# Optimization experiments

Hardware: AMD Instinct MI355X
Metric: run time of the kernel (lower is better)

The kernel has to match this reference:

```python
import jax, jax.numpy as jnp
import numpy as np

K = 20      # kNN neighbors
H = 4       # attention heads
EPS = 1e-5  # BatchNorm eps
NEG = 0.2   # LeakyReLU negative slope


def lrelu(x):
    return jnp.where(x >= 0, x, NEG * x)


def bn(x, g, b):
    # eval-mode BatchNorm: running_mean=0, running_var=1
    return x * (g / jnp.sqrt(1.0 + EPS)) + b


def knn_idx(x):
    # x: (B, N, C) -> (B, N, K) indices of K nearest neighbors (incl. self)
    inner = -2.0 * jnp.einsum('bnc,bmc->bnm', x, x)
    xx = jnp.sum(x * x, axis=-1)
    pd = -xx[:, :, None] - inner - xx[:, None, :]  # negative squared distance
    return jax.lax.top_k(pd, K)[1]


def edge_conv(x, w, g, b):
    # EdgeConv: gather kNN features, cat(nbr-ctr, ctr), 1x1 conv, BN, LeakyReLU, max over K
    idx = knn_idx(x)                                   # (B,N,K)
    nbr = jax.vmap(lambda f, i: f[i])(x, idx)          # (B,N,K,C)
    ctr = jnp.broadcast_to(x[:, :, None, :], nbr.shape)
    e = jnp.concatenate([nbr - ctr, ctr], axis=-1)     # (B,N,K,2C)
    h = lrelu(bn(jnp.einsum('bnkc,oc->bnko', e, w), g, b))
    return jnp.max(h, axis=2)                          # (B,N,Cout)


def mha(x, w_in, b_in, w_out, b_out):
    # Faithful to source: (B,N,E) fed to nn.MultiheadAttention with batch_first=False,
    # so seq length L=B and batch=N (attention mixes across the batch axis).
    L, Nb, E = x.shape
    d = E // H
    qkv = x @ w_in.T + b_in
    q, k, v = jnp.split(qkv, 3, axis=-1)
    q = q.reshape(L, Nb, H, d) * (1.0 / np.sqrt(d))
    k = k.reshape(L, Nb, H, d)
    v = v.reshape(L, Nb, H, d)
    a = jax.nn.softmax(jnp.einsum('lnhd,mnhd->nhlm', q, k), axis=-1)
    o = jnp.einsum('nhlm,mnhd->lnhd', a, v).reshape(L, Nb, E)
    return o @ w_out.T + b_out


def setup_inputs():
    ks = iter(jax.random.split(jax.random.key(0), 64))
    def rn(shape, s=0.05):
        return jax.random.normal(next(ks), shape, jnp.float32) * s
    def gamma(c):
        return 1.0 + rn((c,), 0.1)
    B, N = 8, 1024
    inp = {'x': rn((B, N, 3), 1.0)}
    for i, (ci, co) in enumerate([(6, 64), (128, 64), (128, 128), (256, 256)], 1):
        inp[f'w{i}'] = rn((co, ci)); inp[f'g{i}'] = gamma(co); inp[f'b{i}'] = rn((co,))
    for i, e in enumerate([64, 64, 128, 256], 1):
        inp[f'a{i}_wi'] = rn((3 * e, e)); inp[f'a{i}_bi'] = rn((3 * e,))
        inp[f'a{i}_wo'] = rn((e, e));     inp[f'a{i}_bo'] = rn((e,))
    inp['w5'] = rn((1024, 512)); inp['g5'] = gamma(1024); inp['b5'] = rn((1024,))
    inp['l1w'] = rn((512, 2048)); inp['g6'] = gamma(512); inp['b6'] = rn((512,))
    inp['l2w'] = rn((256, 512)); inp['l2b'] = rn((256,))
    inp['g7'] = gamma(256); inp['b7'] = rn((256,))
    inp['l3w'] = rn((40, 256)); inp['l3b'] = rn((40,))
    return inp


def reference(x, w1, g1, b1, a1_wi, a1_bi, a1_wo, a1_bo,
              w2, g2, b2, a2_wi, a2_bi, a2_wo, a2_bo,
              w3, g3, b3, a3_wi, a3_bi, a3_wo, a3_bo,
              w4, g4, b4, a4_wi, a4_bi, a4_wo, a4_bo,
              w5, g5, b5, l1w, g6, b6, l2w, l2b, g7, b7, l3w, l3b):
    x1 = edge_conv(x, w1, g1, b1)
    x1 = mha(x1, a1_wi, a1_bi, a1_wo, a1_bo) + x1
    x2 = edge_conv(x1, w2, g2, b2)
    x2 = mha(x2, a2_wi, a2_bi, a2_wo, a2_bo) + x2
    x3 = edge_conv(x2, w3, g3, b3)
    x3 = mha(x3, a3_wi, a3_bi, a3_wo, a3_bo) + x3
    x4 = edge_conv(x3, w4, g4, b4)
    x4 = mha(x4, a4_wi, a4_bi, a4_wo, a4_bo) + x4
    h = lrelu(bn(jnp.concatenate([x1, x2, x3, x4], axis=-1) @ w5.T, g5, b5))  # (B,N,1024)
    feat = jnp.concatenate([jnp.max(h, axis=1), jnp.mean(h, axis=1)], axis=-1)  # (B,2048)
    h = lrelu(bn(feat @ l1w.T, g6, b6))
    h = lrelu(bn(h @ l2w.T + l2b, g7, b7))  # dropout is eval-mode identity
    return h @ l3w.T + l3b  # (B, 40)
```

## Files before the change

### kernel.cpp

```cpp
#include <hip/hip_runtime.h>
#include <hip/hip_bf16.h>

#define B_ 8
#define N_ 1024
#define K_ 20
#define BN_ (B_*N_)

#define BN_SCALE 0.9999950000374997f

typedef __attribute__((ext_vector_type(8))) short short8;
typedef __attribute__((ext_vector_type(4))) float f32x4;

__device__ __forceinline__ float US2F(unsigned short u) {
    union { unsigned u; float f; } c; c.u = ((unsigned)u) << 16; return c.f;
}
__device__ __forceinline__ unsigned short F2BF(float f) {
    union { float f; unsigned u; } c; c.f = f;
    unsigned r = c.u + 0x7FFF + ((c.u >> 16) & 1);
    return (unsigned short)(r >> 16);
}

__device__ __forceinline__ void ldsld16(const unsigned short* g, unsigned short* l) {
    __builtin_amdgcn_global_load_lds(
        (const __attribute__((address_space(1))) void*)g,
        (__attribute__((address_space(3))) void*)l, 16, 0, 0);
}

struct DetP { const unsigned short* g[7]; };
__device__ __forceinline__ int det_isbf(const DetP& dp) {
    int cnt = 0;
    #pragma unroll
    for (int i = 0; i < 7; i++) {
        float v = US2F(dp.g[i][0]);
        if (v > 0.5f && v < 1.5f) cnt++;
    }
    return cnt >= 4;
}

struct TPar { const void* src; void* dst; int O, I, blk0, mode; };
struct TList { TPar p[44]; };
struct TrP { const void* src; float* dst; int O, I, bx, blk0; };

__global__ __launch_bounds__(256) void k_prep(TList tl, int nent,
                                              TrP q0, TrP q1, TrP q2,
                                              int nbp, int nbtr,
                                              const void* x0, DetP dp,
                                              unsigned short* __restrict__ xa,
                                              unsigned short* __restrict__ xb,
                                              float* __restrict__ xx1) {
    __shared__ int sbf;
    if (threadIdx.x == 0) sbf = det_isbf(dp);
    __syncthreads();
    const int isbf = sbf;
    auto ld0 = [&](int idx) {
        return isbf ? US2F(((const unsigned short*)x0)[idx])
                    : ((const float*)x0)[idx];
    };
    const int bid = blockIdx.x;
    if (bid >= nbp + nbtr) {
        int blk = bid - nbp - nbtr;
        if (blk >= (BN_ * 32) / 256) {
            int i = (blk - (BN_ * 32) / 256) * 256 + threadIdx.x;
            if (i >= BN_) return;
            float s = 0.f;
            #pragma unroll
            for (int c = 0; c < 3; c++) { float v = ld0(i * 3 + c); s += v * v; }
            xx1[i] = s;
            return;
        }
        const int e = blk * 256 + threadIdx.x;
        const int i = e >> 5, p = e & 31;
        unsigned short va = 0, vb = 0;
        if (p < 9) {
            const int seg = p / 3, c = p - seg * 3;
            const float v = ld0(i * 3 + c);
            const unsigned short h = F2BF(v);
            const unsigned short l = F2BF(v - US2F(h));
            va = (seg == 1) ? l : h;
            vb = (seg < 2) ? h : l;
        }
        xa[e] = va; xb[e] = vb;
        return;
    }
    if (bid >= nbp) {
        int blk = bid - nbp;
        TrP p = q0;
        if (blk >= q2.blk0) p = q2; else if (blk >= q1.blk0) p = q1;
        blk -= p.blk0;
        const int tx = threadIdx.x & 31, ty = threadIdx.x >> 5;
        const int bi = blk % p.bx, bo = blk / p.bx;
        const int i0 = bi * 32, o0 = bo * 32;
        __shared__ float s[32][33];
        #pragma unroll
        for (int r = 0; r < 4; r++) {
            const int o = o0 + ty + r * 8, i = i0 + tx;
            if (o < p.O && i < p.I) {
                const size_t e = (size_t)o * p.I + i;
                s[ty + r * 8][tx] = isbf ? US2F(((const unsigned short*)p.src)[e])
                                         : ((const float*)p.src)[e];
            }
        }
        __syncthreads();
        #pragma unroll
        for (int r = 0; r < 4; r++) {
            const int i = i0 + ty + r * 8, o = o0 + tx;
            if (i < p.I && o < p.O) p.dst[(size_t)i * p.O + o] = s[tx][ty + r * 8];
        }
        return;
    }
    int blk = bid;
    int wi = 0;
    for (int j = nent - 1; j >= 0; j--) { if (blk >= tl.p[j].blk0) { wi = j; break; } }
    const TPar p = tl.p[wi];
    int e = (blk - p.blk0) * 256 + threadIdx.x;
    int n = p.O * p.I;
    if (e >= n) return;
    if (p.mode == 4) { ((float*)p.dst)[e] = 0.f; return; }
    int o = e / p.I, i = e - o * p.I;
    float v = isbf ? US2F(((const unsigned short*)p.src)[e])
                   : ((const float*)p.src)[e];
    if (p.mode == 0) {
        ((float*)p.dst)[(size_t)i * p.O + o] = v;
    } else if (p.mode == 2) {
        ((unsigned short*)p.dst)[e] = F2BF(v);
    } else {
        const int C = p.I >> 1;
        if (i < C) ((unsigned short*)p.dst)[(size_t)o * C + i] = F2BF(v);
        else       ((unsigned short*)p.dst)[(size_t)(p.O + o) * C + (i - C)] = F2BF(v);
    }
}

template<int KP, int TM, int TN>
__global__ __launch_bounds__(256) void k_pdm(const unsigned short* __restrict__ xa,
                                             const unsigned short* __restrict__ xb,
                                             const float* __restrict__ xx,
                                             float* __restrict__ pd) {
    const int bid = blockIdx.x;
    const int b = bid & 7;
    const int tt = bid >> 3;
    const int rb = (tt >> 3) * TM, cb = (tt & 7) * TN;
    const unsigned short* Ab = xa + (size_t)b * N_ * KP;
    const unsigned short* Bb = xb + (size_t)b * N_ * KP;
    const float* xxb = xx + (size_t)b * N_;
    const int t = threadIdx.x;
    __shared__ __align__(16) unsigned short As[2][TM * 32];
    __shared__ __align__(16) unsigned short Bs[2][TN * 32];
    const int w = t >> 6, lane = t & 63;
    constexpr int QR = TM / 2, QC = TN / 2;
    constexpr int MR = QR / 16, NR = QC / 16;
    const int wr = (w & 1) * QR, wc = (w >> 1) * QC;
    const int fr = lane & 15, q = lane >> 4;
    f32x4 acc[MR][NR] = {};

    auto STAGE = [&](int buf, int k0) {
        constexpr int AT = TM * 4;
        #pragma unroll
        for (int R = 0; R < (AT + 255) / 256; R++) {
            const int G = t + R * 256;
            if (AT >= (R + 1) * 256 || G < AT) {
                const int m = G >> 2, gs = (G & 3) ^ ((m >> 1) & 3);
                ldsld16(&Ab[(size_t)(rb + m) * KP + k0 + gs * 8], &As[buf][w * 512 + R * 2048]);
            }
        }
        constexpr int BT = TN * 4;
        #pragma unroll
        for (int R = 0; R < (BT + 255) / 256; R++) {
            const int G = t + R * 256;
            if (BT >= (R + 1) * 256 || G < BT) {
                const int n = G >> 2, gs = (G & 3) ^ ((n >> 1) & 3);
                ldsld16(&Bb[(size_t)(cb + n) * KP + k0 + gs * 8], &Bs[buf][w * 512 + R * 2048]);
            }
        }
    };

    constexpr int NT = KP / 32;
    STAGE(0, 0);
    asm volatile("s_waitcnt vmcnt(0)" ::: "memory");
    __builtin_amdgcn_s_barrier();
    int cur = 0;
    for (int ts = 0; ts < NT; ++ts) {
        if (ts + 1 < NT) STAGE(cur ^ 1, (ts + 1) * 32);
        short8 af[MR], bfr[NR];
        #pragma unroll
        for (int mi = 0; mi < MR; mi++) {
            const int r = wr + mi * 16 + fr;
            af[mi] = *reinterpret_cast<const short8*>(&As[cur][r * 32 + ((q ^ ((r >> 1) & 3)) << 3)]);
        }
        #pragma unroll
        for (int ni = 0; ni < NR; ni++) {
            const int r = wc + ni * 16 + fr;
            bfr[ni] = *reinterpret_cast<const short8*>(&Bs[cur][r * 32 + ((q ^ ((r >> 1) & 3)) << 3)]);
        }
        #pragma unroll
        for (int mi = 0; mi < MR; mi++) {
            #pragma unroll
            for (int ni = 0; ni < NR; ni++)
                acc[mi][ni] = __builtin_amdgcn_mfma_f32_16x16x32_bf16(af[mi], bfr[ni], acc[mi][ni], 0, 0, 0);
        }
        asm volatile("s_waitcnt vmcnt(0)" ::: "memory");
        __builtin_amdgcn_s_barrier();
        cur ^= 1;
    }
    float* pdb = pd + (size_t)b * N_ * N_;
    const int cr = (lane >> 4) * 4, cc = lane & 15;
    #pragma unroll
    for (int mi = 0; mi < MR; mi++) {
        #pragma unroll
        for (int ni = 0; ni < NR; ni++) {
            #pragma unroll
            for (int r = 0; r < 4; r++) {
                const int row = rb + wr + mi * 16 + cr + r;
                const int col = cb + wc + ni * 16 + cc;
                pdb[(size_t)row * N_ + col] = 2.f * acc[mi][ni][r] - xxb[col];
            }
        }
    }
}

__device__ __forceinline__ void sel_dev(const float* __restrict__ pd,
                                        int* __restrict__ idx, int blk) {
    const int w = threadIdx.x >> 6, lane = threadIdx.x & 63;
    const int b = blk & 7;
    const int i = (b << 10) + ((blk >> 3) << 2) + w;
    const float* row = pd + (size_t)b * N_ * N_ + (size_t)(i & 1023) * N_;
    unsigned key[16];
    #pragma unroll
    for (int q = 0; q < 16; q++) {
        const int j = q * 64 + lane;
        unsigned bits = __float_as_uint(row[j]);
        bits = (bits & 0x80000000u) ? ~bits : (bits | 0x80000000u);
        key[q] = (bits & 0xFFFFFC00u) | (unsigned)(N_ - 1 - j);
    }
    int myj = 0;
    for (int kk = 0; kk < K_; kk++) {
        unsigned m = key[0];
        #pragma unroll
        for (int u = 1; u < 16; u++) m = key[u] > m ? key[u] : m;
        #pragma unroll
        for (int s = 1; s < 64; s <<= 1) {
            unsigned o = (unsigned)__shfl_xor((int)m, s, 64);
            m = o > m ? o : m;
        }
        const int j = N_ - 1 - (int)(m & 1023u);
        if (lane == kk) myj = j;
        #pragma unroll
        for (int u = 0; u < 16; u++)
            if (key[u] == m) key[u] = 0u;
    }
    if (lane < K_) idx[(size_t)i * K_ + lane] = myj;
}

template<int KD, int NC, int TM, int TN, bool CATA, bool POOL, int SPLIT>
__device__ __forceinline__ void gemm_dev(int bx, int by,
                                         const unsigned short* __restrict__ A,
                                         const unsigned short* __restrict__ A2,
                                         const unsigned short* __restrict__ A3,
                                         const unsigned short* __restrict__ A4,
                                         const unsigned short* __restrict__ Bw,
                                         const float* __restrict__ bias,
                                         const float* __restrict__ resid,
                                         float* __restrict__ Cout,
                                         float* __restrict__ Cz, int yco,
                                         int scale_cols, float qs,
                                         const float* __restrict__ gamma,
                                         const float* __restrict__ beta,
                                         unsigned short* __restrict__ obf,
                                         unsigned* __restrict__ pmaxu,
                                         float* __restrict__ psum,
                                         unsigned short* __restrict__ sxa,
                                         unsigned short* __restrict__ sxb,
                                         float* __restrict__ xxo) {
    const int t = threadIdx.x;
    const int rb = bx * TM, cb = by * TN;
    const int w = t >> 6, lane = t & 63;
    constexpr int QR = TM / 2, QC = TN / 2;
    constexpr int MR = QR / 16, NR = QC / 16;
    const int wr = (w & 1) * QR, wc = (w >> 1) * QC;
    const int fr = lane & 15, q = lane >> 4, fq = q * 8;
    f32x4 acc[MR][NR] = {};
    if constexpr (KD % 32 == 0) {
        __shared__ __align__(16) unsigned short As[2][TM * 32];
        __shared__ __align__(16) unsigned short Bs[2][TN * 32];
        auto STAGE = [&](int buf, int k0) {
            const unsigned short* Asrc = A; int AC = KD, ac0 = k0;
            if constexpr (CATA) {
                if (k0 >= 256)      { Asrc = A4; AC = 256; ac0 = k0 - 256; }
                else if (k0 >= 128) { Asrc = A3; AC = 128; ac0 = k0 - 128; }
                else if (k0 >= 64)  { Asrc = A2; AC = 64;  ac0 = k0 - 64; }
                else                { Asrc = A;  AC = 64;  ac0 = k0; }
            }
            constexpr int AT = TM * 4;
            #pragma unroll
            for (int R = 0; R < (AT + 255) / 256; R++) {
                const int G = t + R * 256;
                if (AT >= (R + 1) * 256 || G < AT) {
                    const int m = G >> 2, gs = (G & 3) ^ ((m >> 1) & 3);
                    ldsld16(&Asrc[(size_t)(rb + m) * AC + ac0 + gs * 8], &As[buf][w * 512 + R * 2048]);
                }
            }
            constexpr int BT = TN * 4;
            #pragma unroll
            for (int R = 0; R < (BT + 255) / 256; R++) {
                const int G = t + R * 256;
                if (BT >= (R + 1) * 256 || G < BT) {
                    const int n = G >> 2, gs = (G & 3) ^ ((n >> 1) & 3);
                    ldsld16(&Bw[(size_t)(cb + n) * KD + k0 + gs * 8], &Bs[buf][w * 512 + R * 2048]);
                }
            }
        };
        constexpr int NT = KD / 32;
        STAGE(0, 0);
        asm volatile("s_waitcnt vmcnt(0)" ::: "memory");
        __builtin_amdgcn_s_barrier();
        int cur = 0;
        for (int ts = 0; ts < NT; ++ts) {
            if (ts + 1 < NT) STAGE(cur ^ 1, (ts + 1) * 32);
            short8 af[MR], bfr[NR];
            #pragma unroll
            for (int mi = 0; mi < MR; mi++) {
                const int r = wr + mi * 16 + fr;
                af[mi] = *reinterpret_cast<const short8*>(&As[cur][r * 32 + ((q ^ ((r >> 1) & 3)) << 3)]);
            }
            #pragma unroll
            for (int ni = 0; ni < NR; ni++) {
                const int r = wc + ni * 16 + fr;
                bfr[ni] = *reinterpret_cast<const short8*>(&Bs[cur][r * 32 + ((q ^ ((r >> 1) & 3)) << 3)]);
            }
            #pragma unroll
            for (int mi = 0; mi < MR; mi++) {
                #pragma unroll
                for (int ni = 0; ni < NR; ni++)
                    acc[mi][ni] = __builtin_amdgcn_mfma_f32_16x16x32_bf16(af[mi], bfr[ni], acc[mi][ni], 0, 0, 0);
            }
            asm volatile("s_waitcnt vmcnt(0)" ::: "memory");
            __builtin_amdgcn_s_barrier();
            cur ^= 1;
        }
    } else {
        __shared__ __align__(16) unsigned short As[TM * 40];
        __shared__ __align__(16) unsigned short Bs[TN * 40];
        for (int k0 = 0; k0 < KD; k0 += 32) {
            __syncthreads();
            #pragma unroll
            for (int u = t; u < TM * 4; u += 256) {
                const int m = u >> 2, c = (u & 3) * 8;
                #pragma unroll
                for (int j = 0; j < 8; j++) {
                    const int kk = k0 + c + j;
                    As[m * 40 + c + j] = (kk < KD) ? A[(size_t)(rb + m) * KD + kk] : (unsigned short)0;
                }
            }
            #pragma unroll
            for (int u = t; u < TN * 4; u += 256) {
                const int n = u >> 2, c = (u & 3) * 8;
                const int gn = cb + n;
                if (gn < NC) {
                    #pragma unroll
                    for (int j = 0; j < 8; j++) {
                        const int kk = k0 + c + j;
                        Bs[n * 40 + c + j] = (kk < KD) ? Bw[(size_t)gn * KD + kk] : (unsigned short)0;
                    }
                } else {
                    short8 z = {};
                    *reinterpret_cast<short8*>(&Bs[n * 40 + c]) = z;
                }
            }
            __syncthreads();
            short8 af[MR], bfr[NR];
            #pragma unroll
            for (int mi = 0; mi < MR; mi++)
                af[mi] = *reinterpret_cast<const short8*>(&As[(wr + mi * 16 + fr) * 40 + fq]);
            #pragma unroll
            for (int ni = 0; ni < NR; ni++)
                bfr[ni] = *reinterpret_cast<const short8*>(&Bs[(wc + ni * 16 + fr) * 40 + fq]);
            #pragma unroll
            for (int mi = 0; mi < MR; mi++) {
                #pragma unroll
                for (int ni = 0; ni < NR; ni++)
                    acc[mi][ni] = __builtin_amdgcn_mfma_f32_16x16x32_bf16(af[mi], bfr[ni], acc[mi][ni], 0, 0, 0);
            }
        }
    }
    const int cr = (lane >> 4) * 4, cc = lane & 15;
    if constexpr (POOL) {
        const int bidx = rb >> 10;
        #pragma unroll
        for (int ni = 0; ni < NR; ni++) {
            const int col = cb + wc + ni * 16 + cc;
            const float gm = gamma[col] * BN_SCALE, bt = beta[col];
            float sm = 0.f, mxv = -3e38f;
            #pragma unroll
            for (int mi = 0; mi < MR; mi++) {
                #pragma unroll
                for (int r = 0; r < 4; r++) {
                    float v = acc[mi][ni][r] * gm + bt;
                    v = v >= 0.f ? v : 0.2f * v;
                    sm += v; mxv = fmaxf(mxv, v);
                }
            }
            sm += __shfl_xor(sm, 16, 64);
            sm += __shfl_xor(sm, 32, 64);
            mxv = fmaxf(mxv, __shfl_xor(mxv, 16, 64));
            mxv = fmaxf(mxv, __shfl_xor(mxv, 32, 64));
            if (lane < 16) {
                atomicAdd(&psum[bidx * 1024 + col], sm);
                unsigned tb = __float_as_uint(mxv);
                tb = (tb & 0x80000000u) ? ~tb : (tb | 0x80000000u);
                atomicMax(&pmaxu[bidx * 1024 + col], tb);
            }
        }
    } else {
        float sx[MR][4] = {};
        #pragma unroll
        for (int mi = 0; mi < MR; mi++) {
            #pragma unroll
            for (int ni = 0; ni < NR; ni++) {
                #pragma unroll
                for (int r = 0; r < 4; r++) {
                    const int row = rb + wr + mi * 16 + cr + r;
                    const int col = cb + wc + ni * 16 + cc;
                    if (col < NC) {
                        float v = acc[mi][ni][r] + (bias ? bias[col] : 0.f);
                        if (col < scale_cols) v *= qs;
                        if (resid) v += resid[(size_t)row * NC + col];
                        if (gamma) {
                            v = v * (gamma[col] * BN_SCALE) + beta[col];
                            v = v >= 0.f ? v : 0.2f * v;
                        }
                        if (yco > 0) {
                            if (col < yco) Cout[(size_t)row * yco + col] = v;
                            else           Cz[(size_t)row * yco + (col - yco)] = v;
                        } else {
                            Cout[(size_t)row * NC + col] = v;
                        }
                        if (obf) obf[(size_t)row * NC + col] = F2BF(v);
                        if constexpr (SPLIT > 0) {
                            constexpr int KP2 = 3 * SPLIT;
                            const unsigned short h = F2BF(v);
                            const unsigned short l = F2BF(v - US2F(h));
                            sxa[(size_t)row * KP2 + 0 * SPLIT + col] = h;
                            sxa[(size_t)row * KP2 + 1 * SPLIT + col] = l;
                            sxa[(size_t)row * KP2 + 2 * SPLIT + col] = h;
                            sxb[(size_t)row * KP2 + 0 * SPLIT + col] = h;
                            sxb[(size_t)row * KP2 + 1 * SPLIT + col] = h;
                            sxb[(size_t)row * KP2 + 2 * SPLIT + col] = l;
                            sx[mi][r] += v * v;
                        }
                    }
                }
            }
        }
        if constexpr (SPLIT > 0) {
            #pragma unroll
            for (int mi = 0; mi < MR; mi++) {
                #pragma unroll
                for (int r = 0; r < 4; r++) {
                    float s = sx[mi][r];
                    s += __shfl_xor(s, 1, 64);
                    s += __shfl_xor(s, 2, 64);
                    s += __shfl_xor(s, 4, 64);
                    s += __shfl_xor(s, 8, 64);
                    if ((lane & 15) == 0)
                        atomicAdd(&xxo[rb + wr + mi * 16 + cr + r], s);
                }
            }
        }
    }
}

template<int KD, int NC, int TM, int TN, bool CATA = false, bool POOL = false, int SPLIT = 0, bool AFF = false>
__global__ __launch_bounds__(256) void k_gemmb(const unsigned short* __restrict__ A,
                                               const unsigned short* __restrict__ A2,
                                               const unsigned short* __restrict__ A3,
                                               const unsigned short* __restrict__ A4,
                                               const unsigned short* __restrict__ Bw,
                                               const float* __restrict__ bias,
                                               const float* __restrict__ resid,
                                               float* __restrict__ Cout,
                                               int scale_cols, float qs,
                                               const float* __restrict__ gamma,
                                               const float* __restrict__ beta,
                                               unsigned short* __restrict__ obf,
                                               unsigned* __restrict__ pmaxu,
                                               float* __restrict__ psum,
                                               unsigned short* __restrict__ sxa,
                                               unsigned short* __restrict__ sxb,
                                               float* __restrict__ xxo) {
    int bx = blockIdx.x;
    if constexpr (AFF) bx = (bx & 7) * (gridDim.x >> 3) + (bx >> 3);
    gemm_dev<KD, NC, TM, TN, CATA, POOL, SPLIT>(bx, blockIdx.y,
        A, A2, A3, A4, Bw, bias, resid, Cout, nullptr, 0, scale_cols, qs, gamma, beta,
        obf, pmaxu, psum, sxa, sxb, xxo);
}

template<int KD, int NC, int TM, int TN>
__global__ __launch_bounds__(256) void k_selyz(const float* __restrict__ pd,
                                               int* __restrict__ idx, int selb, int gx,
                                               const unsigned short* __restrict__ A,
                                               const unsigned short* __restrict__ Bw,
                                               float* __restrict__ Cy,
                                               float* __restrict__ Cz, int yco) {
    if ((int)blockIdx.x < selb) { sel_dev(pd, idx, blockIdx.x); return; }
    const int g = blockIdx.x - selb;
    const int batch = g & 7, rem = g >> 3;
    const int rpb = gx >> 3;
    const int bx = batch * rpb + rem % rpb;
    const int by = rem / rpb;
    gemm_dev<KD, NC, TM, TN, false, false, 0>(bx, by,
        A, nullptr, nullptr, nullptr, Bw, nullptr, nullptr, Cy, Cz, yco, 0, 1.f,
        nullptr, nullptr, nullptr, nullptr, nullptr, nullptr, nullptr, nullptr);
}

template<int CO>
__global__ __launch_bounds__(256) void k_edgemax(const float* __restrict__ y,
                                                 const float* __restrict__ z,
                                                 const int* __restrict__ idx,
                                                 const float* __restrict__ g,
                                                 const float* __restrict__ bb,
                                                 float* __restrict__ out,
                                                 unsigned short* __restrict__ outb) {
    constexpr int TPP = CO / 4;
    constexpr int PPB = 256 / TPP;
    const int t = threadIdx.x;
    const int p = t / TPP;
    const int cw = (t % TPP) * 4;
    const int batch = blockIdx.x & 7;
    const int within = blockIdx.x >> 3;
    const int i0 = batch * N_ + within * PPB;
    const int bbase = batch << 10;
    __shared__ int sidx[PPB][K_];
    for (int u = t; u < PPB * K_; u += 256) {
        int pp = u / K_, kk = u - pp * K_;
        sidx[pp][kk] = idx[(size_t)(i0 + pp) * K_ + kk];
    }
    __syncthreads();
    const int ig = i0 + p;
    float4 m = {-3e38f, -3e38f, -3e38f, -3e38f};
    #pragma unroll 4
    for (int k = 0; k < K_; k++) {
        const int jg = bbase + sidx[p][k];
        const float4 yv = *reinterpret_cast<const float4*>(&y[(size_t)jg * CO + cw]);
        m.x = fmaxf(m.x, yv.x); m.y = fmaxf(m.y, yv.y);
        m.z = fmaxf(m.z, yv.z); m.w = fmaxf(m.w, yv.w);
    }
    const float4 yi = *reinterpret_cast<const float4*>(&y[(size_t)ig * CO + cw]);
    const float4 zi = *reinterpret_cast<const float4*>(&z[(size_t)ig * CO + cw]);
    const float4 gv = *reinterpret_cast<const float4*>(&g[cw]);
    const float4 bv = *reinterpret_cast<const float4*>(&bb[cw]);
    float vals[4] = {m.x - yi.x + zi.x, m.y - yi.y + zi.y,
                     m.z - yi.z + zi.z, m.w - yi.w + zi.w};
    float gs[4] = {gv.x, gv.y, gv.z, gv.w};
    float bs[4] = {bv.x, bv.y, bv.z, bv.w};
    float4 o;
    float* op = &o.x;
    #pragma unroll
    for (int j = 0; j < 4; j++) {
        float h = vals[j] * (gs[j] * BN_SCALE) + bs[j];
        op[j] = h >= 0.f ? h : 0.2f * h;
    }
    *reinterpret_cast<float4*>(&out[(size_t)ig * CO + cw]) = o;
    #pragma unroll
    for (int j = 0; j < 4; j++) outb[(size_t)ig * CO + cw + j] = F2BF(op[j]);
}

template<int E>
__global__ __launch_bounds__(256) void k_attn(const float* __restrict__ qkv,
                                              unsigned short* __restrict__ o) {
    constexpr int H = 4, D = E / H, L = 8;
    const int n = blockIdx.x;
    const int t = threadIdx.x;
    const int h = t >> 6, lane = t & 63;
    __shared__ float sq[L][3 * E];
    __shared__ float so[L][E];
    for (int u = t; u < L * 3 * E; u += 256) {
        int l = u / (3 * E), r = u - l * (3 * E);
        sq[l][r] = qkv[(size_t)(l * N_ + n) * (3 * E) + r];
    }
    __syncthreads();
    const int l = lane >> 3, m = lane & 7;
    float s = 0.f;
    #pragma unroll 8
    for (int dd = 0; dd < D; dd++)
        s += sq[l][h * D + dd] * sq[m][E + h * D + dd];
    float mx = s;
    #pragma unroll
    for (int st = 1; st < 8; st <<= 1) mx = fmaxf(mx, __shfl_xor(mx, st, 64));
    float e = expf(s - mx);
    float sum = e;
    #pragma unroll
    for (int st = 1; st < 8; st <<= 1) sum += __shfl_xor(sum, st, 64);
    const float p = e / sum;
    float pm[8];
    #pragma unroll
    for (int mm = 0; mm < 8; mm++) pm[mm] = __shfl(p, (lane & 56) | mm, 64);
    #pragma unroll
    for (int j = 0; j < D / 8; j++) {
        const int dd = m + 8 * j;
        float a = 0.f;
        #pragma unroll
        for (int mm = 0; mm < 8; mm++) a += pm[mm] * sq[mm][2 * E + h * D + dd];
        so[l][h * D + dd] = a;
    }
    __syncthreads();
    for (int u = t; u < L * E; u += 256) {
        int l2 = u / E, e2 = u - l2 * E;
        o[(size_t)(l2 * N_ + n) * E + e2] = F2BF(so[l2][e2]);
    }
}

__global__ __launch_bounds__(256) void k_fc1(const unsigned* __restrict__ pmaxu,
                                             const float* __restrict__ psum,
                                             const float* __restrict__ l1wT,
                                             const float* __restrict__ g6, const float* __restrict__ b6,
                                             float* __restrict__ f1) {
    int oc = blockIdx.x, b = blockIdx.y, t = threadIdx.x;
    __shared__ float fin[2048];
    __shared__ float ps[4][64];
    for (int u = t; u < 2048; u += 256) {
        float v;
        if (u < 1024) {
            unsigned tb = pmaxu[b * 1024 + u];
            unsigned bits = (tb & 0x80000000u) ? (tb & 0x7FFFFFFFu) : ~tb;
            v = __uint_as_float(bits);
        } else {
            v = psum[b * 1024 + (u - 1024)] * (1.f / 1024.f);
        }
        fin[u] = v;
    }
    __syncthreads();
    int ol = t & 63, kc = t >> 6;
    int o = oc * 64 + ol;
    float acc = 0.f;
    for (int c = kc * 512; c < kc * 512 + 512; c++) acc += fin[c] * l1wT[(size_t)c * 512 + o];
    ps[kc][ol] = acc;
    __syncthreads();
    if (t < 64) {
        int oo = oc * 64 + t;
        float a = ps[0][t] + ps[1][t] + ps[2][t] + ps[3][t];
        float h = a * (g6[oo] * BN_SCALE) + b6[oo];
        f1[b * 512 + oo] = h >= 0.f ? h : 0.2f * h;
    }
}

__global__ __launch_bounds__(256) void k_fc23(const float* __restrict__ f1, const float* __restrict__ l2wT,
                                              const float* __restrict__ l2b,
                                              const float* __restrict__ g7, const float* __restrict__ b7,
                                              const float* __restrict__ l3wT, const float* __restrict__ l3b,
                                              void* __restrict__ out, DetP dp) {
    int b = blockIdx.x, t = threadIdx.x;
    __shared__ float fin[512];
    __shared__ float f2s[256];
    __shared__ int sbf;
    if (t == 0) sbf = det_isbf(dp);
    for (int u = t; u < 512; u += 256) fin[u] = f1[b * 512 + u];
    __syncthreads();
    {
        float acc = 0.f;
        for (int c = 0; c < 512; c++) acc += fin[c] * l2wT[(size_t)c * 256 + t];
        acc += l2b[t];
        float h = acc * (g7[t] * BN_SCALE) + b7[t];
        f2s[t] = h >= 0.f ? h : 0.2f * h;
    }
    __syncthreads();
    if (t < 40) {
        float acc = 0.f;
        for (int c = 0; c < 256; c++) acc += f2s[c] * l3wT[(size_t)c * 40 + t];
        acc += l3b[t];
        if (sbf) ((__hip_bfloat16*)out)[b * 40 + t] = __float2bfloat16(acc);
        else     ((float*)out)[b * 40 + t] = acc;
    }
}

extern "C" void kernel_launch(void* const* d_in, const int* in_sizes, int n_in,
                              void* d_out, int out_size, void* d_ws, size_t ws_size,
                              hipStream_t stream) {
    auto us = [&](int i) { return (const unsigned short*)d_in[i]; };

    float* ws = (float*)d_ws;
    size_t off = 0;
    auto A = [&](size_t n) { float* p = ws + off; off += (n + 3) & ~(size_t)3; return p; };
    auto AU = [&](size_t n) { return (unsigned short*)A((n + 1) / 2); };
    float* x1   = A((size_t)BN_ * 64);
    float* x2   = A((size_t)BN_ * 64);
    float* x3   = A((size_t)BN_ * 128);
    float* x4   = A((size_t)BN_ * 256);
    float* pd   = A((size_t)BN_ * 1024);
    float* f1   = A(8 * 512);
    float* xx   = A(4 * BN_);
    int*   idx  = (int*)A((size_t)BN_ * K_);
    float* qkvw = A((size_t)BN_ * 768);
    unsigned short* xf0b = AU((size_t)BN_ * 3);
    unsigned short* x1b  = AU((size_t)BN_ * 64);
    unsigned short* x2b  = AU((size_t)BN_ * 64);
    unsigned short* x3b  = AU((size_t)BN_ * 128);
    unsigned short* x4b  = AU((size_t)BN_ * 256);
    unsigned short* owb  = AU((size_t)BN_ * 256);
    unsigned* pmaxu = (unsigned*)A(8 * 1024);
    float*    psum  = A(8 * 1024);
    unsigned short* w1yzb = AU(128 * 3);
    unsigned short* w2yzb = AU(128 * 64);
    unsigned short* w3yzb = AU(256 * 64);
    unsigned short* w4yzb = AU(512 * 128);
    unsigned short* a1wib = AU(192 * 64);  unsigned short* a1wob = AU(64 * 64);
    unsigned short* a2wib = AU(192 * 64);  unsigned short* a2wob = AU(64 * 64);
    unsigned short* a3wib = AU(384 * 128); unsigned short* a3wob = AU(128 * 128);
    unsigned short* a4wib = AU(768 * 256); unsigned short* a4wob = AU(256 * 256);
    unsigned short* w5b   = AU(1024 * 512);
    float* l1wT  = A(2048 * 512);
    float* l2wT  = A(512 * 256);
    float* l3wT  = A(256 * 40);
    float* g1f = A(64);   float* b1f = A(64);
    float* g2f = A(64);   float* b2f = A(64);
    float* g3f = A(128);  float* b3f = A(128);
    float* g4f = A(256);  float* b4f = A(256);
    float* bi1 = A(192);  float* bo1 = A(64);
    float* bi2 = A(192);  float* bo2 = A(64);
    float* bi3 = A(384);  float* bo3 = A(128);
    float* bi4 = A(768);  float* bo4 = A(256);
    float* g5f = A(1024); float* b5f = A(1024);
    float* g6f = A(512);  float* b6f = A(512);
    float* l2bf = A(256);
    float* g7f = A(256);  float* b7f = A(256);
    float* l3bf = A(40);

    float* xx1 = xx;              float* xx2 = xx + BN_;
    float* xx3 = xx + 2 * BN_;    float* xx4 = xx + 3 * BN_;

    unsigned short* xa = (unsigned short*)qkvw;
    unsigned short* xb = (unsigned short*)qkvw + (size_t)BN_ * 384;
    float* yy = qkvw;
    float* zz = qkvw + (size_t)BN_ * 256;

    DetP dp{{us(2), us(5), us(8), us(11), us(30), us(33), us(37)}};

    TList tl; int nb = 0; int k = 0;
    auto add = [&](int i, void* dst, int O, int I, int mode) {
        tl.p[k].src = d_in[i]; tl.p[k].dst = dst; tl.p[k].O = O; tl.p[k].I = I;
        tl.p[k].blk0 = nb; tl.p[k].mode = mode;
        nb += (O * I + 255) / 256; k++;
    };
    add(0,  xf0b,  BN_ * 3, 1, 2);
    add(0,  pmaxu, 16384, 1, 4);
    add(0,  xx2,   3 * BN_, 1, 4);
    add(1,  w1yzb, 64, 6, 3);
    add(4,  w2yzb, 64, 128, 3);
    add(7,  w3yzb, 128, 128, 3);
    add(10, w4yzb, 256, 256, 3);
    add(13, a1wib, 192, 64, 2);
    add(15, a1wob, 64, 64, 2);
    add(17, a2wib, 192, 64, 2);
    add(19, a2wob, 64, 64, 2);
    add(21, a3wib, 384, 128, 2);
    add(23, a3wob, 128, 128, 2);
    add(25, a4wib, 768, 256, 2);
    add(27, a4wob, 256, 256, 2);
    add(29, w5b,   1024, 512, 2);
    add(2,  g1f, 64, 1, 0);   add(3,  b1f, 64, 1, 0);
    add(5,  g2f, 64, 1, 0);   add(6,  b2f, 64, 1, 0);
    add(8,  g3f, 128, 1, 0);  add(9,  b3f, 128, 1, 0);
    add(11, g4f, 256, 1, 0);  add(12, b4f, 256, 1, 0);
    add(14, bi1, 192, 1, 0);  add(16, bo1, 64, 1, 0);
    add(18, bi2, 192, 1, 0);  add(20, bo2, 64, 1, 0);
    add(22, bi3, 384, 1, 0);  add(24, bo3, 128, 1, 0);
    add(26, bi4, 768, 1, 0);  add(28, bo4, 256, 1, 0);
    add(30, g5f, 1024, 1, 0); add(31, b5f, 1024, 1, 0);
    add(33, g6f, 512, 1, 0);  add(34, b6f, 512, 1, 0);
    add(36, l2bf, 256, 1, 0);
    add(37, g7f, 256, 1, 0);  add(38, b7f, 256, 1, 0);
    add(40, l3bf, 40, 1, 0);

    TrP tp1{d_in[32], l1wT, 512, 2048, 2048 / 32, 0};
    TrP tp2{d_in[35], l2wT, 256, 512,  512 / 32,  (2048 / 32) * (512 / 32)};
    TrP tp3{d_in[39], l3wT, 40,  256,  256 / 32,  tp2.blk0 + (512 / 32) * (256 / 32)};
    const int trblocks = tp3.blk0 + (256 / 32) * ((40 + 31) / 32);
    const int splblocks = (BN_ * 32) / 256 + 32;
    k_prep<<<nb + trblocks + splblocks, 256, 0, stream>>>(
        tl, k, tp1, tp2, tp3, nb, trblocks, d_in[0], dp, xa, xb, xx1);

    const unsigned short* N0 = nullptr;
    unsigned short* U0 = nullptr;
    unsigned* NU = nullptr; float* NF = nullptr;

    k_pdm<32, 128, 128><<<512, 256, 0, stream>>>(xa, xb, xx1, pd);
    k_selyz<3, 128, 64, 64><<<2048 + 256, 256, 0, stream>>>(pd, idx, 2048, 128, xf0b, w1yzb, yy, zz, 64);
    k_edgemax<64><<<BN_ / 16, 256, 0, stream>>>(yy, zz, idx, g1f, b1f, x1, x1b);
    k_gemmb<64, 192, 64, 64, false, false, 0, true><<<dim3(128, 3), 256, 0, stream>>>(x1b, N0, N0, N0, a1wib, bi1, nullptr, qkvw, 64, 0.25f, nullptr, nullptr, nullptr, NU, NF, U0, U0, NF);
    k_attn<64><<<N_, 256, 0, stream>>>(qkvw, owb);
    k_gemmb<64, 64, 64, 64, false, false, 64, true><<<dim3(128, 1), 256, 0, stream>>>(owb, N0, N0, N0, a1wob, bo1, x1, x1, 0, 1.f, nullptr, nullptr, x1b, NU, NF, xa, xb, xx2);

    k_pdm<192, 128, 128><<<512, 256, 0, stream>>>(xa, xb, xx2, pd);
    k_selyz<64, 128, 64, 64><<<2048 + 256, 256, 0, stream>>>(pd, idx, 2048, 128, x1b, w2yzb, yy, zz, 64);
    k_edgemax<64><<<BN_ / 16, 256, 0, stream>>>(yy, zz, idx, g2f, b2f, x2, x2b);
    k_gemmb<64, 192, 64, 64, false, false, 0, true><<<dim3(128, 3), 256, 0, stream>>>(x2b, N0, N0, N0, a2wib, bi2, nullptr, qkvw, 64, 0.25f, nullptr, nullptr, nullptr, NU, NF, U0, U0, NF);
    k_attn<64><<<N_, 256, 0, stream>>>(qkvw, owb);
    k_gemmb<64, 64, 64, 64, false, false, 64, true><<<dim3(128, 1), 256, 0, stream>>>(owb, N0, N0, N0, a2wob, bo2, x2, x2, 0, 1.f, nullptr, nullptr, x2b, NU, NF, xa, xb, xx3);

    k_pdm<192, 128, 128><<<512, 256, 0, stream>>>(xa, xb, xx3, pd);
    k_selyz<64, 256, 64, 64><<<2048 + 512, 256, 0, stream>>>(pd, idx, 2048, 128, x2b, w3yzb, yy, zz, 128);
    k_edgemax<128><<<BN_ / 8, 256, 0, stream>>>(yy, zz, idx, g3f, b3f, x3, x3b);
    k_gemmb<128, 384, 64, 128, false, false, 0, true><<<dim3(128, 3), 256, 0, stream>>>(x3b, N0, N0, N0, a3wib, bi3, nullptr, qkvw, 128, 0.17677669529663687f, nullptr, nullptr, nullptr, NU, NF, U0, U0, NF);
    k_attn<128><<<N_, 256, 0, stream>>>(qkvw, owb);
    k_gemmb<128, 128, 64, 64, false, false, 128, true><<<dim3(128, 2), 256, 0, stream>>>(owb, N0, N0, N0, a3wob, bo3, x3, x3, 0, 1.f, nullptr, nullptr, x3b, NU, NF, xa, xb, xx4);

    k_pdm<384, 128, 128><<<512, 256, 0, stream>>>(xa, xb, xx4, pd);
    k_selyz<128, 512, 128, 128><<<2048 + 256, 256, 0, stream>>>(pd, idx, 2048, 64, x3b, w4yzb, yy, zz, 256);
    k_edgemax<256><<<BN_ / 4, 256, 0, stream>>>(yy, zz, idx, g4f, b4f, x4, x4b);
    k_gemmb<256, 768, 64, 128, false, false, 0, true><<<dim3(128, 6), 256, 0, stream>>>(x4b, N0, N0, N0, a4wib, bi4, nullptr, qkvw, 256, 0.125f, nullptr, nullptr, nullptr, NU, NF, U0, U0, NF);
    k_attn<256><<<N_, 256, 0, stream>>>(qkvw, owb);
    k_gemmb<256, 256, 64, 128, false, false, 0, true><<<dim3(128, 2), 256, 0, stream>>>(owb, N0, N0, N0, a4wob, bo4, x4, x4, 0, 1.f, nullptr, nullptr, x4b, NU, NF, U0, U0, NF);

    k_gemmb<512, 1024, 128, 128, true, true, 0, true><<<dim3(64, 8), 256, 0, stream>>>(
        x1b, x2b, x3b, x4b, w5b, nullptr, nullptr, nullptr, 0, 1.f, g5f, b5f, nullptr, pmaxu, psum, U0, U0, NF);
    k_fc1<<<dim3(8, 8), 256, 0, stream>>>(pmaxu, psum, l1wT, g6f, b6f, f1);
    k_fc23<<<8, 256, 0, stream>>>(f1, l2wT, l2bf, g7f, b7f, l3wT, l3bf, d_out, dp);
}
```

Baseline: 501.7 us.

## Fuse attention with output projection and residual for first three layers

Adds a k_attnout kernel that computes the cross-batch softmax attention for one point and then applies the output projection, bias, residual add, bf16 conversion, hi/lo split for the next kNN and squared-norm accumulation, all in the same block. This replaces the separate k_attn and k_gemmb launches for layers 1-3 and drops the owb round trip through global memory. xa/xb get their own workspace because they can no longer alias qkvw, which is still being read. The output projection now runs as scalar FMAs from LDS instead of the MFMA GEMM, and each block reloads the full E×E weight matrix, so redundant weight traffic and slower math may offset the saved launches.

```diff
diff --git a/kernel.cpp b/kernel.cpp
--- a/kernel.cpp
+++ b/kernel.cpp
@@ -608,6 +608,93 @@
     }
 }
 
+template<int E, int SPLIT>
+__global__ __launch_bounds__(256) void k_attnout(const float* __restrict__ qkv,
+                                                 const unsigned short* __restrict__ wo,
+                                                 const float* __restrict__ bo,
+                                                 float* __restrict__ x,
+                                                 unsigned short* __restrict__ xob,
+                                                 unsigned short* __restrict__ sxa,
+                                                 unsigned short* __restrict__ sxb,
+                                                 float* __restrict__ xxo) {
+    constexpr int H = 4, D = E / H, L = 8;
+    const int n = blockIdx.x;
+    const int t = threadIdx.x;
+    const int h = t >> 6, lane = t & 63;
+    __shared__ float sq[L][3 * E];
+    __shared__ float so[L][E];
+    __shared__ unsigned short swo[E][E + 8];
+    __shared__ float sxx[L];
+    for (int u = t; u < L * 3 * E; u += 256) {
+        int l = u / (3 * E), r = u - l * (3 * E);
+        sq[l][r] = qkv[(size_t)(l * N_ + n) * (3 * E) + r];
+    }
+    for (int u = t; u < E * E; u += 256) swo[u / E][u % E] = wo[u];
+    if (t < L) sxx[t] = 0.f;
+    __syncthreads();
+    const int l = lane >> 3, m = lane & 7;
+    float s = 0.f;
+    #pragma unroll 8
+    for (int dd = 0; dd < D; dd++)
+        s += sq[l][h * D + dd] * sq[m][E + h * D + dd];
+    float mx = s;
+    #pragma unroll
+    for (int st = 1; st < 8; st <<= 1) mx = fmaxf(mx, __shfl_xor(mx, st, 64));
+    float e = expf(s - mx);
+    float sum = e;
+    #pragma unroll
+    for (int st = 1; st < 8; st <<= 1) sum += __shfl_xor(sum, st, 64);
+    const float p = e / sum;
+    float pm[8];
+    #pragma unroll
+    for (int mm = 0; mm < 8; mm++) pm[mm] = __shfl(p, (lane & 56) | mm, 64);
+    #pragma unroll
+    for (int j = 0; j < D / 8; j++) {
+        const int dd = m + 8 * j;
+        float a = 0.f;
+        #pragma unroll
+        for (int mm = 0; mm < 8; mm++) a += pm[mm] * sq[mm][2 * E + h * D + dd];
+        so[l][h * D + dd] = a;
+    }
+    __syncthreads();
+    for (int u = t; u < L * E; u += 256)
+        so[u / E][u % E] = US2F(F2BF(so[u / E][u % E]));
+    __syncthreads();
+    constexpr int PT = (L * E) / 256;
+    #pragma unroll
+    for (int it = 0; it < PT; it++) {
+        const int item = t + it * 256;
+        const int ll = item / E, ee = item % E;
+        float acc = 0.f;
+        #pragma unroll 16
+        for (int c = 0; c < E; c++)
+            acc += so[ll][c] * US2F(swo[ee][c]);
+        const int row = ll * N_ + n;
+        const float v = acc + bo[ee] + x[(size_t)row * E + ee];
+        x[(size_t)row * E + ee] = v;
+        xob[(size_t)row * E + ee] = F2BF(v);
+        if constexpr (SPLIT > 0) {
+            constexpr int KP2 = 3 * SPLIT;
+            const unsigned short hh = F2BF(v);
+            const unsigned short lo = F2BF(v - US2F(hh));
+            sxa[(size_t)row * KP2 + 0 * SPLIT + ee] = hh;
+            sxa[(size_t)row * KP2 + 1 * SPLIT + ee] = lo;
+            sxa[(size_t)row * KP2 + 2 * SPLIT + ee] = hh;
+            sxb[(size_t)row * KP2 + 0 * SPLIT + ee] = hh;
+            sxb[(size_t)row * KP2 + 1 * SPLIT + ee] = hh;
+            sxb[(size_t)row * KP2 + 2 * SPLIT + ee] = lo;
+            float vs = v * v;
+            #pragma unroll
+            for (int st = 1; st < 64; st <<= 1) vs += __shfl_xor(vs, st, 64);
+            if (lane == 0) atomicAdd(&sxx[ll], vs);
+        }
+    }
+    if constexpr (SPLIT > 0) {
+        __syncthreads();
+        if (t < L) xxo[t * N_ + n] = sxx[t];
+    }
+}
+
 __global__ __launch_bounds__(256) void k_fc1(const unsigned* __restrict__ pmaxu,
                                              const float* __restrict__ psum,
                                              const float* __restrict__ l1wT,
@@ -689,6 +776,8 @@
     float* xx   = A(4 * BN_);
     int*   idx  = (int*)A((size_t)BN_ * K_);
     float* qkvw = A((size_t)BN_ * 768);
+    unsigned short* xa = AU((size_t)BN_ * 384);
+    unsigned short* xb = AU((size_t)BN_ * 384);
     unsigned short* xf0b = AU((size_t)BN_ * 3);
     unsigned short* x1b  = AU((size_t)BN_ * 64);
     unsigned short* x2b  = AU((size_t)BN_ * 64);
@@ -726,8 +815,6 @@
     float* xx1 = xx;              float* xx2 = xx + BN_;
     float* xx3 = xx + 2 * BN_;    float* xx4 = xx + 3 * BN_;
 
-    unsigned short* xa = (unsigned short*)qkvw;
-    unsigned short* xb = (unsigned short*)qkvw + (size_t)BN_ * 384;
     float* yy = qkvw;
     float* zz = qkvw + (size_t)BN_ * 256;
 
@@ -741,7 +828,6 @@
     };
     add(0,  xf0b,  BN_ * 3, 1, 2);
     add(0,  pmaxu, 16384, 1, 4);
-    add(0,  xx2,   3 * BN_, 1, 4);
     add(1,  w1yzb, 64, 6, 3);
     add(4,  w2yzb, 64, 128, 3);
     add(7,  w3yzb, 128, 128, 3);
@@ -785,22 +871,19 @@
     k_selyz<3, 128, 64, 64><<<2048 + 256, 256, 0, stream>>>(pd, idx, 2048, 128, xf0b, w1yzb, yy, zz, 64);
     k_edgemax<64><<<BN_ / 16, 256, 0, stream>>>(yy, zz, idx, g1f, b1f, x1, x1b);
     k_gemmb<64, 192, 64, 64, false, false, 0, true><<<dim3(128, 3), 256, 0, stream>>>(x1b, N0, N0, N0, a1wib, bi1, nullptr, qkvw, 64, 0.25f, nullptr, nullptr, nullptr, NU, NF, U0, U0, NF);
-    k_attn<64><<<N_, 256, 0, stream>>>(qkvw, owb);
-    k_gemmb<64, 64, 64, 64, false, false, 64, true><<<dim3(128, 1), 256, 0, stream>>>(owb, N0, N0, N0, a1wob, bo1, x1, x1, 0, 1.f, nullptr, nullptr, x1b, NU, NF, xa, xb, xx2);
+    k_attnout<64, 64><<<N_, 256, 0, stream>>>(qkvw, a1wob, bo1, x1, x1b, xa, xb, xx2);
 
     k_pdm<192, 128, 128><<<512, 256, 0, stream>>>(xa, xb, xx2, pd);
     k_selyz<64, 128, 64, 64><<<2048 + 256, 256, 0, stream>>>(pd, idx, 2048, 128, x1b, w2yzb, yy, zz, 64);
     k_edgemax<64><<<BN_ / 16, 256, 0, stream>>>(yy, zz, idx, g2f, b2f, x2, x2b);
     k_gemmb<64, 192, 64, 64, false, false, 0, true><<<dim3(128, 3), 256, 0, stream>>>(x2b, N0, N0, N0, a2wib, bi2, nullptr, qkvw, 64, 0.25f, nullptr, nullptr, nullptr, NU, NF, U0, U0, NF);
-    k_attn<64><<<N_, 256, 0, stream>>>(qkvw, owb);
-    k_gemmb<64, 64, 64, 64, false, false, 64, true><<<dim3(128, 1), 256, 0, stream>>>(owb, N0, N0, N0, a2wob, bo2, x2, x2, 0, 1.f, nullptr, nullptr, x2b, NU, NF, xa, xb, xx3);
+    k_attnout<64, 64><<<N_, 256, 0, stream>>>(qkvw, a2wob, bo2, x2, x2b, xa, xb, xx3);
 
     k_pdm<192, 128, 128><<<512, 256, 0, stream>>>(xa, xb, xx3, pd);
     k_selyz<64, 256, 64, 64><<<2048 + 512, 256, 0, stream>>>(pd, idx, 2048, 128, x2b, w3yzb, yy, zz, 128);
     k_edgemax<128><<<BN_ / 8, 256, 0, stream>>>(yy, zz, idx, g3f, b3f, x3, x3b);
     k_gemmb<128, 384, 64, 128, false, false, 0, true><<<dim3(128, 3), 256, 0, stream>>>(x3b, N0, N0, N0, a3wib, bi3, nullptr, qkvw, 128, 0.17677669529663687f, nullptr, nullptr, nullptr, NU, NF, U0, U0, NF);
-    k_attn<128><<<N_, 256, 0, stream>>>(qkvw, owb);
-    k_gemmb<128, 128, 64, 64, false, false, 128, true><<<dim3(128, 2), 256, 0, stream>>>(owb, N0, N0, N0, a3wob, bo3, x3, x3, 0, 1.f, nullptr, nullptr, x3b, NU, NF, xa, xb, xx4);
+    k_attnout<128, 128><<<N_, 256, 0, stream>>>(qkvw, a3wob, bo3, x3, x3b, xa, xb, xx4);
 
     k_pdm<384, 128, 128><<<512, 256, 0, stream>>>(xa, xb, xx4, pd);
     k_selyz<128, 512, 128, 128><<<2048 + 256, 256, 0, stream>>>(pd, idx, 2048, 64, x3b, w4yzb, yy, zz, 256);
```

New measurement: 486.4 us. 3.1% less time.
